# Kernel tuning notes

Measured on AMD Instinct MI355X. Metric: run time of the kernel, lower is better.

## Reference

```python
import jax, jax.numpy as jnp
import numpy as np

B, V, J = 16384, 8, 21  # batch, views, joints (J=21 hard-coded in LAT)


def setup_inputs() -> dict:
    key = jax.random.key(0)
    k1, k2, k3, k4 = jax.random.split(key, 4)
    intrinsic = jax.random.normal(k1, (B, V, 3, 3), dtype=jnp.float32)
    extrinsic = jax.random.normal(k2, (B, V, 3, 4), dtype=jnp.float32)
    # uv ~ pixel coordinates in [0, 256)
    uv = jax.random.uniform(k3, (B, V, J, 2), dtype=jnp.float32) * 256.0
    confidences = jax.random.uniform(k4, (B, V, J), dtype=jnp.float32)
    return {"intrinsic": intrinsic, "extrinsic": extrinsic, "uv": uv,
            "confidences": confidences}


def reference(intrinsic, extrinsic, uv, confidences):
    # Projection matrices P = K @ [R|T]: (B,V,3,4)
    P = jnp.einsum('bvij,bvjk->bvik', intrinsic, extrinsic)
    Pj = P[:, :, None]                      # (B,V,1,3,4), broadcast over joints
    u = uv[..., 0:1]                        # (B,V,J,1)
    v = uv[..., 1:2]                        # (B,V,J,1)
    w = confidences[..., None]              # (B,V,J,1)
    # Weighted DLT rows: (B,V,J,4)
    row0 = w * (u * Pj[..., 2, :] - Pj[..., 0, :])
    row1 = w * (v * Pj[..., 2, :] - Pj[..., 1, :])
    A = jnp.stack([row0, row1], axis=3)     # (B,V,J,2,4)
    A = A.transpose(0, 2, 1, 3, 4).reshape(B * J, 2 * V, 4)  # (BJ, 2V, 4)
    # Smallest right singular vector of each (2V,4) system
    _, _, Vh = jnp.linalg.svd(A, full_matrices=False)  # Vh: (BJ,4,4)
    X_homo = Vh[:, -1, :]                   # (BJ, 4)
    w_homo = X_homo[:, 3:4]                 # (BJ, 1)
    total_w = confidences.sum(axis=1).reshape(B * J, 1)
    valid = ((total_w > 0.1) & (jnp.abs(w_homo) > 1e-6)).astype(X_homo.dtype)
    X_3d = X_homo[:, :3] / (w_homo + 1e-8) * valid
    return X_3d.reshape(B, J, 3)
```

## Files before the change

### kernel.cpp

```cpp
#include <hip/hip_runtime.h>
#include <math.h>

constexpr int B = 16384;
constexpr int V = 8;
constexpr int J = 21;


__device__ __forceinline__ double fast_rsqrt(double u) {
    double r = (double)__builtin_amdgcn_rsqf((float)u);
    double hu = -0.5 * u;
    r = r * fma(hu * r, r, 1.5);
    return r;
}

#define PSTAGE(app, aqq, apq, arr, ass, ars, ca, cb, cd, ce,               \
               v0p, v0q, v1p, v1q, v2p, v2q, v3p, v3q,                     \
               w0r, w0s, w1r, w1s, w2r, w2s, w3r, w3s)                     \
  {                                                                        \
    double dA_ = aqq - app;                                                \
    double uA_ = fma(dA_, dA_, 4.0 * (apq * apq));                         \
    double riA_ = fast_rsqrt(uA_);                                         \
    double c2A_ = fma(0.5 * fabs(dA_), riA_, 0.5);                         \
    double icA_ = fast_rsqrt(c2A_);                                        \
    double cA_ = c2A_ * icA_;                                              \
    double sA_ = ((dA_ >= 0.0) ? apq : -apq) * (riA_ * icA_);              \
    double tA_ = sA_ * icA_;                                               \
    bool zA_ = (apq == 0.0);                                               \
    cA_ = zA_ ? 1.0 : cA_; sA_ = zA_ ? 0.0 : sA_; tA_ = zA_ ? 0.0 : tA_;   \
    double dB_ = ass - arr;                                                \
    double uB_ = fma(dB_, dB_, 4.0 * (ars * ars));                         \
    double riB_ = fast_rsqrt(uB_);                                         \
    double c2B_ = fma(0.5 * fabs(dB_), riB_, 0.5);                         \
    double icB_ = fast_rsqrt(c2B_);                                        \
    double cB_ = c2B_ * icB_;                                              \
    double sB_ = ((dB_ >= 0.0) ? ars : -ars) * (riB_ * icB_);              \
    double tB_ = sB_ * icB_;                                               \
    bool zB_ = (ars == 0.0);                                               \
    cB_ = zB_ ? 1.0 : cB_; sB_ = zB_ ? 0.0 : sB_; tB_ = zB_ ? 0.0 : tB_;   \
    double tpA_ = tA_ * apq; app -= tpA_; aqq += tpA_; apq = 0.0;          \
    double tpB_ = tB_ * ars; arr -= tpB_; ass += tpB_; ars = 0.0;          \
    double a_ = ca, b_ = cb, d_ = cd, e_ = ce;                             \
    double a1_ = fma(cA_, a_, -sA_ * d_), d1_ = fma(sA_, a_, cA_ * d_);    \
    double b1_ = fma(cA_, b_, -sA_ * e_), e1_ = fma(sA_, b_, cA_ * e_);    \
    ca = fma(cB_, a1_, -sB_ * b1_); cb = fma(sB_, a1_, cB_ * b1_);         \
    cd = fma(cB_, d1_, -sB_ * e1_); ce = fma(sB_, d1_, cB_ * e1_);         \
    double x_, y_;                                                         \
    x_ = v0p; y_ = v0q; v0p = fma(cA_, x_, -sA_ * y_); v0q = fma(sA_, x_, cA_ * y_); \
    x_ = v1p; y_ = v1q; v1p = fma(cA_, x_, -sA_ * y_); v1q = fma(sA_, x_, cA_ * y_); \
    x_ = v2p; y_ = v2q; v2p = fma(cA_, x_, -sA_ * y_); v2q = fma(sA_, x_, cA_ * y_); \
    x_ = v3p; y_ = v3q; v3p = fma(cA_, x_, -sA_ * y_); v3q = fma(sA_, x_, cA_ * y_); \
    x_ = w0r; y_ = w0s; w0r = fma(cB_, x_, -sB_ * y_); w0s = fma(sB_, x_, cB_ * y_); \
    x_ = w1r; y_ = w1s; w1r = fma(cB_, x_, -sB_ * y_); w1s = fma(sB_, x_, cB_ * y_); \
    x_ = w2r; y_ = w2s; w2r = fma(cB_, x_, -sB_ * y_); w2s = fma(sB_, x_, cB_ * y_); \
    x_ = w3r; y_ = w3s; w3r = fma(cB_, x_, -sB_ * y_); w3s = fma(sB_, x_, cB_ * y_); \
  }

__global__ __launch_bounds__(64, 4)
void triangulate_kernel(const float* __restrict__ intr,
                        const float* __restrict__ extr,
                        const float* __restrict__ uv,
                        const float* __restrict__ conf,
                        float* __restrict__ out)
{
    int t = blockIdx.x * blockDim.x + threadIdx.x;
    if (t >= B * J) return;
    int b = t / J;
    int j = t - b * J;

    double m00 = 0, m01 = 0, m02 = 0, m03 = 0;
    double m11 = 0, m12 = 0, m13 = 0;
    double m22 = 0, m23 = 0;
    double m33 = 0;
    float total_w = 0.0f;

    for (int v = 0; v < V; ++v) {
        const float* Kp = intr + (size_t)(b * V + v) * 9;
        const float* Ep = extr + (size_t)(b * V + v) * 12;
        float K0 = Kp[0], K1 = Kp[1], K2 = Kp[2];
        float K3 = Kp[3], K4 = Kp[4], K5 = Kp[5];
        float K6 = Kp[6], K7 = Kp[7], K8 = Kp[8];

        float P0[4], P1[4], P2[4];
        #pragma unroll
        for (int k = 0; k < 4; ++k) {
            float e0 = Ep[k], e1 = Ep[4 + k], e2 = Ep[8 + k];
            P0[k] = fmaf(K0, e0, fmaf(K1, e1, __fmul_rn(K2, e2)));
            P1[k] = fmaf(K3, e0, fmaf(K4, e1, __fmul_rn(K5, e2)));
            P2[k] = fmaf(K6, e0, fmaf(K7, e1, __fmul_rn(K8, e2)));
        }

        size_t uvbase = (size_t)(b * V + v) * J + j;
        float uu = uv[uvbase * 2 + 0];
        float vv = uv[uvbase * 2 + 1];
        float w  = conf[uvbase];
        total_w += w;

        float r0[4], r1[4];
        #pragma unroll
        for (int k = 0; k < 4; ++k) {
            r0[k] = __fmul_rn(w, fmaf(uu, P2[k], -P0[k]));
            r1[k] = __fmul_rn(w, fmaf(vv, P2[k], -P1[k]));
        }

        m00 += (double)r0[0] * r0[0] + (double)r1[0] * r1[0];
        m01 += (double)r0[0] * r0[1] + (double)r1[0] * r1[1];
        m02 += (double)r0[0] * r0[2] + (double)r1[0] * r1[2];
        m03 += (double)r0[0] * r0[3] + (double)r1[0] * r1[3];
        m11 += (double)r0[1] * r0[1] + (double)r1[1] * r1[1];
        m12 += (double)r0[1] * r0[2] + (double)r1[1] * r1[2];
        m13 += (double)r0[1] * r0[3] + (double)r1[1] * r1[3];
        m22 += (double)r0[2] * r0[2] + (double)r1[2] * r1[2];
        m23 += (double)r0[2] * r0[3] + (double)r1[2] * r1[3];
        m33 += (double)r0[3] * r0[3] + (double)r1[3] * r1[3];
    }

    double v00 = 1, v01 = 0, v02 = 0, v03 = 0;
    double v10 = 0, v11 = 1, v12 = 0, v13 = 0;
    double v20 = 0, v21 = 0, v22 = 1, v23 = 0;
    double v30 = 0, v31 = 0, v32 = 0, v33 = 1;

    for (int sweep = 0; sweep < 8; ++sweep) {
        PSTAGE(m00, m11, m01,  m22, m33, m23,  m02, m03, m12, m13,
               v00, v01, v10, v11, v20, v21, v30, v31,
               v02, v03, v12, v13, v22, v23, v32, v33);
        PSTAGE(m00, m22, m02,  m11, m33, m13,  m01, m03, m12, m23,
               v00, v02, v10, v12, v20, v22, v30, v32,
               v01, v03, v11, v13, v21, v23, v31, v33);
        PSTAGE(m00, m33, m03,  m11, m22, m12,  m01, m02, m13, m23,
               v00, v03, v10, v13, v20, v23, v30, v33,
               v01, v02, v11, v12, v21, v22, v31, v32);

        double off2 = m01*m01 + m02*m02 + m03*m03
                    + m12*m12 + m13*m13 + m23*m23;
        double tr = m00 + m11 + m22 + m33;
        if (__all(off2 <= 1e-26 * tr * tr)) break;
    }

    double be = m00;
    double x0 = v00, x1 = v10, x2 = v20, x3 = v30;
    if (m11 < be) { be = m11; x0 = v01; x1 = v11; x2 = v21; x3 = v31; }
    if (m22 < be) { be = m22; x0 = v02; x1 = v12; x2 = v22; x3 = v32; }
    if (m33 < be) { be = m33; x0 = v03; x1 = v13; x2 = v23; x3 = v33; }

    float xw = (float)x3;
    bool valid = (total_w > 0.1f) && (fabsf(xw) > 1e-6f);
    float denom = xw + 1e-8f;
    float o0 = valid ? (float)x0 / denom : 0.0f;
    float o1 = valid ? (float)x1 / denom : 0.0f;
    float o2 = valid ? (float)x2 / denom : 0.0f;

    out[(size_t)t * 3 + 0] = o0;
    out[(size_t)t * 3 + 1] = o1;
    out[(size_t)t * 3 + 2] = o2;
}

extern "C" void kernel_launch(void* const* d_in, const int* in_sizes, int n_in,
                              void* d_out, int out_size, void* d_ws, size_t ws_size,
                              hipStream_t stream) {
    const float* intr = (const float*)d_in[0];
    const float* extr = (const float*)d_in[1];
    const float* uv   = (const float*)d_in[2];
    const float* conf = (const float*)d_in[3];
    float* out = (float*)d_out;

    int total = B * J;
    int block = 64;
    int grid = (total + block - 1) / block;
    triangulate_kernel<<<grid, block, 0, stream>>>(intr, extr, uv, conf, out);
}
```

Baseline: 35.54 us.

## Add two FP32-rotation Jacobi sweeps before FP64 sweeps and loosen convergence tolerance

Adds two unrolled Jacobi sweeps before the FP64 loop. They compute the rotation angles in FP32 and update the diagonal and off-diagonal entries with the full rotation formula, not the zero-the-pivot shortcut. The FP64 loop then starts from a nearly diagonal matrix, and its convergence threshold is loosened from 1e-26 to 1e-18. The aim is to cut the number of costly FP64 sweeps and the rsqrt refinement work, at the risk of slightly less accurate eigenvectors for ill-conditioned systems.

```diff
diff --git a/kernel.cpp b/kernel.cpp
--- a/kernel.cpp
+++ b/kernel.cpp
@@ -55,6 +55,73 @@
     x_ = w3r; y_ = w3s; w3r = fma(cB_, x_, -sB_ * y_); w3s = fma(sB_, x_, cB_ * y_); \
   }
 
+#define F32STAGE(app, aqq, apq, arr, ass, ars, ca, cb, cd, ce,             \
+                 v0p, v0q, v1p, v1q, v2p, v2q, v3p, v3q,                   \
+                 w0r, w0s, w1r, w1s, w2r, w2s, w3r, w3s)                   \
+  {                                                                        \
+    float dfA = (float)(aqq - app);                                        \
+    float afA = (float)(apq);                                              \
+    float ufA = fmaf(dfA, dfA, 4.0f * (afA * afA));                        \
+    float riA = __builtin_amdgcn_rsqf(ufA);                                \
+    float c2A = fmaf(0.5f * fabsf(dfA), riA, 0.5f);                        \
+    float icA = __builtin_amdgcn_rsqf(c2A);                                \
+    float cfA = c2A * icA;                                                 \
+    float sfA = ((dfA >= 0.0f) ? afA : -afA) * (riA * icA);                \
+    bool zA_ = (ufA < 1e-30f);                                             \
+    double cA_ = zA_ ? 1.0 : (double)cfA;                                  \
+    double sA_ = zA_ ? 0.0 : (double)sfA;                                  \
+    float dfB = (float)(ass - arr);                                        \
+    float afB = (float)(ars);                                              \
+    float ufB = fmaf(dfB, dfB, 4.0f * (afB * afB));                        \
+    float riB = __builtin_amdgcn_rsqf(ufB);                                \
+    float c2B = fmaf(0.5f * fabsf(dfB), riB, 0.5f);                        \
+    float icB = __builtin_amdgcn_rsqf(c2B);                                \
+    float cfB = c2B * icB;                                                 \
+    float sfB = ((dfB >= 0.0f) ? afB : -afB) * (riB * icB);                \
+    bool zB_ = (ufB < 1e-30f);                                             \
+    double cB_ = zB_ ? 1.0 : (double)cfB;                                  \
+    double sB_ = zB_ ? 0.0 : (double)sfB;                                  \
+                     \
+    double ccA = cA_ * cA_, ssA = sA_ * sA_, csA = cA_ * sA_;              \
+    double d0A = app - aqq;                                                \
+    double nppA = fma(ccA, app, fma(ssA, aqq, -2.0 * csA * apq));          \
+    double nqqA = fma(ssA, app, fma(ccA, aqq,  2.0 * csA * apq));          \
+    double npqA = fma(csA, d0A, (ccA - ssA) * apq);                        \
+    app = nppA; aqq = nqqA; apq = npqA;                                    \
+                                                               \
+    double ccB = cB_ * cB_, ssB = sB_ * sB_, csB = cB_ * sB_;              \
+    double d0B = arr - ass;                                                \
+    double nppB = fma(ccB, arr, fma(ssB, ass, -2.0 * csB * ars));          \
+    double nqqB = fma(ssB, arr, fma(ccB, ass,  2.0 * csB * ars));          \
+    double npqB = fma(csB, d0B, (ccB - ssB) * ars);                        \
+    arr = nppB; ass = nqqB; ars = npqB;                                    \
+                       \
+    double a_ = ca, b_ = cb, d_ = cd, e_ = ce;                             \
+    double a1_ = fma(cA_, a_, -sA_ * d_), d1_ = fma(sA_, a_, cA_ * d_);    \
+    double b1_ = fma(cA_, b_, -sA_ * e_), e1_ = fma(sA_, b_, cA_ * e_);    \
+    ca = fma(cB_, a1_, -sB_ * b1_); cb = fma(sB_, a1_, cB_ * b1_);         \
+    cd = fma(cB_, d1_, -sB_ * e1_); ce = fma(sB_, d1_, cB_ * e1_);         \
+    double x_, y_;                                                         \
+    x_ = v0p; y_ = v0q; v0p = fma(cA_, x_, -sA_ * y_); v0q = fma(sA_, x_, cA_ * y_); \
+    x_ = v1p; y_ = v1q; v1p = fma(cA_, x_, -sA_ * y_); v1q = fma(sA_, x_, cA_ * y_); \
+    x_ = v2p; y_ = v2q; v2p = fma(cA_, x_, -sA_ * y_); v2q = fma(sA_, x_, cA_ * y_); \
+    x_ = v3p; y_ = v3q; v3p = fma(cA_, x_, -sA_ * y_); v3q = fma(sA_, x_, cA_ * y_); \
+    x_ = w0r; y_ = w0s; w0r = fma(cB_, x_, -sB_ * y_); w0s = fma(sB_, x_, cB_ * y_); \
+    x_ = w1r; y_ = w1s; w1r = fma(cB_, x_, -sB_ * y_); w1s = fma(sB_, x_, cB_ * y_); \
+    x_ = w2r; y_ = w2s; w2r = fma(cB_, x_, -sB_ * y_); w2s = fma(sB_, x_, cB_ * y_); \
+    x_ = w3r; y_ = w3s; w3r = fma(cB_, x_, -sB_ * y_); w3s = fma(sB_, x_, cB_ * y_); \
+  }
+
+#define STAGE1(OP) OP(m00, m11, m01,  m22, m33, m23,  m02, m03, m12, m13,  \
+    v00, v01, v10, v11, v20, v21, v30, v31,                                \
+    v02, v03, v12, v13, v22, v23, v32, v33)
+#define STAGE2(OP) OP(m00, m22, m02,  m11, m33, m13,  m01, m03, m12, m23,  \
+    v00, v02, v10, v12, v20, v22, v30, v32,                                \
+    v01, v03, v11, v13, v21, v23, v31, v33)
+#define STAGE3(OP) OP(m00, m33, m03,  m11, m22, m12,  m01, m02, m13, m23,  \
+    v00, v03, v10, v13, v20, v23, v30, v33,                                \
+    v01, v02, v11, v12, v21, v22, v31, v32)
+
 __global__ __launch_bounds__(64, 4)
 void triangulate_kernel(const float* __restrict__ intr,
                         const float* __restrict__ extr,
@@ -119,21 +186,22 @@
     double v20 = 0, v21 = 0, v22 = 1, v23 = 0;
     double v30 = 0, v31 = 0, v32 = 0, v33 = 1;
 
+    STAGE1(F32STAGE);
+    STAGE2(F32STAGE);
+    STAGE3(F32STAGE);
+    STAGE1(F32STAGE);
+    STAGE2(F32STAGE);
+    STAGE3(F32STAGE);
+
     for (int sweep = 0; sweep < 8; ++sweep) {
-        PSTAGE(m00, m11, m01,  m22, m33, m23,  m02, m03, m12, m13,
-               v00, v01, v10, v11, v20, v21, v30, v31,
-               v02, v03, v12, v13, v22, v23, v32, v33);
-        PSTAGE(m00, m22, m02,  m11, m33, m13,  m01, m03, m12, m23,
-               v00, v02, v10, v12, v20, v22, v30, v32,
-               v01, v03, v11, v13, v21, v23, v31, v33);
-        PSTAGE(m00, m33, m03,  m11, m22, m12,  m01, m02, m13, m23,
-               v00, v03, v10, v13, v20, v23, v30, v33,
-               v01, v02, v11, v12, v21, v22, v31, v32);
+        STAGE1(PSTAGE);
+        STAGE2(PSTAGE);
+        STAGE3(PSTAGE);
 
         double off2 = m01*m01 + m02*m02 + m03*m03
                     + m12*m12 + m13*m13 + m23*m23;
         double tr = m00 + m11 + m22 + m33;
-        if (__all(off2 <= 1e-26 * tr * tr)) break;
+        if (__all(off2 <= 1e-18 * tr * tr)) break;
     }
 
     double be = m00;
```

Result: faster. 33.66 us (-5.3%).
